# Optimization experiments

Hardware: AMD Instinct MI355X
Metric: run time of the kernel (lower is better)

The kernel has to match this reference:

```python
import jax, jax.numpy as jnp
import numpy as np

IN_F = 8192
OUT_F = 8192
MAX_STATES = 100
THRESHOLD = MAX_STATES // 2  # 50


def setup_inputs() -> dict:
    key = jax.random.key(0)
    k1, k2 = jax.random.split(key, 2)
    spike_input = (jax.random.uniform(k1, (IN_F,)) < 0.2).astype(jnp.float32)
    # synapse states as in __init__: randn*5 + threshold, clamped to [1, max_states]
    synapse_states = jnp.clip(
        jax.random.normal(k2, (OUT_F, IN_F)) * 5.0 + THRESHOLD, 1.0, float(MAX_STATES)
    ).astype(jnp.float32)
    membrane_potential = jnp.zeros((OUT_F,), jnp.float32)
    adaptive_threshold = jnp.full((OUT_F,), 3.0, jnp.float32)
    eligibility_trace = jnp.zeros((OUT_F, IN_F), jnp.float32)
    refractory_period = jnp.zeros((OUT_F,), jnp.float32)
    return {
        "spike_input": spike_input,
        "synapse_states": synapse_states,
        "membrane_potential": membrane_potential,
        "adaptive_threshold": adaptive_threshold,
        "eligibility_trace": eligibility_trace,
        "refractory_period": refractory_period,
    }


def reference(spike_input, synapse_states, membrane_potential, adaptive_threshold,
              eligibility_trace, refractory_period):
    # Ternary (effectively binary 0/1) weights from synapse states
    w = (synapse_states > float(THRESHOLD)).astype(jnp.float32)  # [out, in]
    x = spike_input.reshape(-1)                                   # [in]
    current = w @ x                                               # [out]
    # LIF membrane update with refractory gating
    v_mem = membrane_potential * 0.5 + current * (1.0 - refractory_period * 0.5)
    spikes = (v_mem >= adaptive_threshold).astype(jnp.float32)    # [out]
    # Eligibility trace: decay + outer-product accumulation + clamp
    new_trace = jnp.clip(eligibility_trace * 0.8 + jnp.outer(spikes, x), 0.0, 5.0)
    # Refractory update
    new_refractory = jnp.clip(refractory_period + spikes - 0.1, 0.0, 1.0)
    # Membrane reset where spiked
    new_membrane = v_mem * (1.0 - spikes)
    return spikes, new_membrane, new_trace, new_refractory
```

## Files before the change

### kernel.cpp

```cpp
#include <hip/hip_runtime.h>


#define IN_F 8192
#define OUT_F 8192
#define BLOCK 256
#define CHUNKS (IN_F / 4 / 64)

typedef float f32x4 __attribute__((ext_vector_type(4)));

__global__ __launch_bounds__(BLOCK) void snn_fused_kernel(
    const f32x4* __restrict__ x4,
    const float* __restrict__ syn,
    const float* __restrict__ mem,
    const float* __restrict__ thr,
    const float* __restrict__ refr,
    const f32x4* __restrict__ tr4,
    float* __restrict__ out_spikes,
    float* __restrict__ out_mem,
    float* __restrict__ out_refr,
    f32x4* __restrict__ otr4)
{
    const int wave = threadIdx.x >> 6;
    const int lane = threadIdx.x & 63;
    const int row  = (blockIdx.x << 2) + wave;

    const size_t base4 = (size_t)row * (IN_F / 4);
    const f32x4* __restrict__ syn4 = (const f32x4*)syn + base4;

    const float r_in = refr[row];
    const float m_in = mem[row];
    const float t_in = thr[row];

    float acc = 0.0f;
    #pragma unroll 8
    for (int it = 0; it < CHUNKS; ++it) {
        const int idx = (it << 6) + lane;
        const f32x4 s  = __builtin_nontemporal_load(&syn4[idx]);
        const f32x4 xv = x4[idx];
        acc += (s[0] > 50.0f) ? xv[0] : 0.0f;
        acc += (s[1] > 50.0f) ? xv[1] : 0.0f;
        acc += (s[2] > 50.0f) ? xv[2] : 0.0f;
        acc += (s[3] > 50.0f) ? xv[3] : 0.0f;
    }

    #pragma unroll
    for (int off = 32; off > 0; off >>= 1)
        acc += __shfl_xor(acc, off, 64);

    const float v     = m_in * 0.5f + acc * (1.0f - r_in * 0.5f);
    const float spike = (v >= t_in) ? 1.0f : 0.0f;
    if (lane == 0) {
        out_spikes[row] = spike;
        out_mem[row]    = v * (1.0f - spike);
        out_refr[row]   = fminf(fmaxf(r_in + spike - 0.1f, 0.0f), 1.0f);
    }

    #pragma unroll 8
    for (int it = 0; it < CHUNKS; ++it) {
        const int idx = (it << 6) + lane;
        const f32x4 t  = __builtin_nontemporal_load(&tr4[base4 + idx]);
        const f32x4 xv = x4[idx];
        f32x4 o;
        o[0] = fminf(fmaxf(t[0] * 0.8f + spike * xv[0], 0.0f), 5.0f);
        o[1] = fminf(fmaxf(t[1] * 0.8f + spike * xv[1], 0.0f), 5.0f);
        o[2] = fminf(fmaxf(t[2] * 0.8f + spike * xv[2], 0.0f), 5.0f);
        o[3] = fminf(fmaxf(t[3] * 0.8f + spike * xv[3], 0.0f), 5.0f);
        __builtin_nontemporal_store(o, &otr4[base4 + idx]);
    }
}

extern "C" void kernel_launch(void* const* d_in, const int* in_sizes, int n_in,
                              void* d_out, int out_size, void* d_ws, size_t ws_size,
                              hipStream_t stream) {
    const float* x_in  = (const float*)d_in[0];
    const float* syn   = (const float*)d_in[1];
    const float* mem   = (const float*)d_in[2];
    const float* thr   = (const float*)d_in[3];
    const float* trace = (const float*)d_in[4];
    const float* refr  = (const float*)d_in[5];

    float* out = (float*)d_out;
    float* out_spikes = out;
    float* out_mem    = out + OUT_F;
    float* out_trace  = out + 2 * OUT_F;
    float* out_refr   = out + 2 * OUT_F + (size_t)OUT_F * IN_F;

    snn_fused_kernel<<<OUT_F / 4, BLOCK, 0, stream>>>(
        (const f32x4*)x_in, syn, mem, thr, refr,
        (const f32x4*)trace,
        out_spikes, out_mem, out_refr,
        (f32x4*)out_trace);
}
```

Baseline: 578.4 us.

## Process two rows per wave, overlapping second-row dot with first-row trace update

```diff
diff --git a/kernel.cpp b/kernel.cpp
--- a/kernel.cpp
+++ b/kernel.cpp
@@ -4,9 +4,29 @@
 #define IN_F 8192
 #define OUT_F 8192
 #define BLOCK 256
-#define CHUNKS (IN_F / 4 / 64)
+#define ROW4 (IN_F / 4)
+#define CHUNKS (ROW4 / 64)
 
 typedef float f32x4 __attribute__((ext_vector_type(4)));
+
+__device__ __forceinline__ float dot_step(const f32x4 s, const f32x4 xv) {
+    float a = 0.0f;
+    a += (s[0] > 50.0f) ? xv[0] : 0.0f;
+    a += (s[1] > 50.0f) ? xv[1] : 0.0f;
+    a += (s[2] > 50.0f) ? xv[2] : 0.0f;
+    a += (s[3] > 50.0f) ? xv[3] : 0.0f;
+    return a;
+}
+
+__device__ __forceinline__ f32x4 trace_step(const f32x4 t, const f32x4 xv,
+                                            const float spike) {
+    f32x4 o;
+    o[0] = fminf(fmaxf(t[0] * 0.8f + spike * xv[0], 0.0f), 5.0f);
+    o[1] = fminf(fmaxf(t[1] * 0.8f + spike * xv[1], 0.0f), 5.0f);
+    o[2] = fminf(fmaxf(t[2] * 0.8f + spike * xv[2], 0.0f), 5.0f);
+    o[3] = fminf(fmaxf(t[3] * 0.8f + spike * xv[3], 0.0f), 5.0f);
+    return o;
+}
 
 __global__ __launch_bounds__(BLOCK) void snn_fused_kernel(
     const f32x4* __restrict__ x4,
@@ -22,50 +42,64 @@
 {
     const int wave = threadIdx.x >> 6;
     const int lane = threadIdx.x & 63;
-    const int row  = (blockIdx.x << 2) + wave;
+    const int r0   = (blockIdx.x << 3) + (wave << 1);
+    const int r1   = r0 + 1;
 
-    const size_t base4 = (size_t)row * (IN_F / 4);
-    const f32x4* __restrict__ syn4 = (const f32x4*)syn + base4;
+    const f32x4* __restrict__ synA = (const f32x4*)syn + (size_t)r0 * ROW4;
+    const f32x4* __restrict__ synB = (const f32x4*)syn + (size_t)r1 * ROW4;
+    const f32x4* __restrict__ trA  = tr4  + (size_t)r0 * ROW4;
+    const f32x4* __restrict__ trB  = tr4  + (size_t)r1 * ROW4;
+    f32x4* __restrict__ otrA       = otr4 + (size_t)r0 * ROW4;
+    f32x4* __restrict__ otrB       = otr4 + (size_t)r1 * ROW4;
 
-    const float r_in = refr[row];
-    const float m_in = mem[row];
-    const float t_in = thr[row];
+    const float rA = refr[r0], mA = mem[r0], tA = thr[r0];
+    const float rB = refr[r1], mB = mem[r1], tB = thr[r1];
 
-    float acc = 0.0f;
+    float acc0 = 0.0f;
     #pragma unroll 8
     for (int it = 0; it < CHUNKS; ++it) {
         const int idx = (it << 6) + lane;
-        const f32x4 s  = __builtin_nontemporal_load(&syn4[idx]);
-        const f32x4 xv = x4[idx];
-        acc += (s[0] > 50.0f) ? xv[0] : 0.0f;
-        acc += (s[1] > 50.0f) ? xv[1] : 0.0f;
-        acc += (s[2] > 50.0f) ? xv[2] : 0.0f;
-        acc += (s[3] > 50.0f) ? xv[3] : 0.0f;
+        acc0 += dot_step(__builtin_nontemporal_load(&synA[idx]), x4[idx]);
+    }
+    #pragma unroll
+    for (int off = 32; off > 0; off >>= 1)
+        acc0 += __shfl_xor(acc0, off, 64);
+
+    const float v0     = mA * 0.5f + acc0 * (1.0f - rA * 0.5f);
+    const float spike0 = (v0 >= tA) ? 1.0f : 0.0f;
+    if (lane == 0) {
+        out_spikes[r0] = spike0;
+        out_mem[r0]    = v0 * (1.0f - spike0);
+        out_refr[r0]   = fminf(fmaxf(rA + spike0 - 0.1f, 0.0f), 1.0f);
     }
 
+    float acc1 = 0.0f;
+    #pragma unroll 4
+    for (int it = 0; it < CHUNKS; ++it) {
+        const int idx = (it << 6) + lane;
+        const f32x4 xv = x4[idx];
+        const f32x4 s  = __builtin_nontemporal_load(&synB[idx]);
+        const f32x4 t  = __builtin_nontemporal_load(&trA[idx]);
+        acc1 += dot_step(s, xv);
+        __builtin_nontemporal_store(trace_step(t, xv, spike0), &otrA[idx]);
+    }
     #pragma unroll
     for (int off = 32; off > 0; off >>= 1)
-        acc += __shfl_xor(acc, off, 64);
+        acc1 += __shfl_xor(acc1, off, 64);
 
-    const float v     = m_in * 0.5f + acc * (1.0f - r_in * 0.5f);
-    const float spike = (v >= t_in) ? 1.0f : 0.0f;
+    const float v1     = mB * 0.5f + acc1 * (1.0f - rB * 0.5f);
+    const float spike1 = (v1 >= tB) ? 1.0f : 0.0f;
     if (lane == 0) {
-        out_spikes[row] = spike;
-        out_mem[row]    = v * (1.0f - spike);
-        out_refr[row]   = fminf(fmaxf(r_in + spike - 0.1f, 0.0f), 1.0f);
+        out_spikes[r1] = spike1;
+        out_mem[r1]    = v1 * (1.0f - spike1);
+        out_refr[r1]   = fminf(fmaxf(rB + spike1 - 0.1f, 0.0f), 1.0f);
     }
 
     #pragma unroll 8
     for (int it = 0; it < CHUNKS; ++it) {
         const int idx = (it << 6) + lane;
-        const f32x4 t  = __builtin_nontemporal_load(&tr4[base4 + idx]);
-        const f32x4 xv = x4[idx];
-        f32x4 o;
-        o[0] = fminf(fmaxf(t[0] * 0.8f + spike * xv[0], 0.0f), 5.0f);
-        o[1] = fminf(fmaxf(t[1] * 0.8f + spike * xv[1], 0.0f), 5.0f);
-        o[2] = fminf(fmaxf(t[2] * 0.8f + spike * xv[2], 0.0f), 5.0f);
-        o[3] = fminf(fmaxf(t[3] * 0.8f + spike * xv[3], 0.0f), 5.0f);
-        __builtin_nontemporal_store(o, &otr4[base4 + idx]);
+        const f32x4 t  = __builtin_nontemporal_load(&trB[idx]);
+        __builtin_nontemporal_store(trace_step(t, x4[idx], spike1), &otrB[idx]);
     }
 }
 
@@ -85,7 +119,7 @@
     float* out_trace  = out + 2 * OUT_F;
     float* out_refr   = out + 2 * OUT_F + (size_t)OUT_F * IN_F;
 
-    snn_fused_kernel<<<OUT_F / 4, BLOCK, 0, stream>>>(
+    snn_fused_kernel<<<OUT_F / 8, BLOCK, 0, stream>>>(
         (const f32x4*)x_in, syn, mem, thr, refr,
         (const f32x4*)trace,
         out_spikes, out_mem, out_refr,
```

New measurement: 588.2 us. About the same (+1.7%).
